# Kernel tuning notes

Measured on AMD Instinct MI355X. Metric: run time of the kernel, lower is better.

The kernel has to match this reference:

```python
import jax, jax.numpy as jnp
import numpy as np

B, N, C, K, H = 64, 4096, 256, 8, 256  # H = max(dim, hidden_dim=128)
ITERS = 3
EPS = 1e-8


def _ln(x, g, b):
    # torch LayerNorm: biased variance, eps=1e-5
    m = x.mean(-1, keepdims=True)
    v = ((x - m) ** 2).mean(-1, keepdims=True)
    return (x - m) * jax.lax.rsqrt(v + 1e-5) * g + b


def setup_inputs() -> dict:
    key = jax.random.key(0)
    ks = jax.random.split(key, 16)
    s = 0.02
    d = {}
    d['inputs'] = jax.random.normal(ks[0], (B, N, C), jnp.float32)
    d['slots_noise'] = jax.random.normal(ks[1], (K, C), jnp.float32)  # eval-mode shared noise
    d['mu'] = jax.random.normal(ks[2], (C,), jnp.float32)
    d['log_sigma'] = jax.random.normal(ks[3], (C,), jnp.float32) * 0.1
    d['ln_in_g'] = jnp.ones((C,), jnp.float32); d['ln_in_b'] = jnp.zeros((C,), jnp.float32)
    d['ln_s_g'] = jnp.ones((C,), jnp.float32); d['ln_s_b'] = jnp.zeros((C,), jnp.float32)
    d['ln_ff_g'] = jnp.ones((C,), jnp.float32); d['ln_ff_b'] = jnp.zeros((C,), jnp.float32)
    d['Wq'] = jax.random.normal(ks[4], (C, C), jnp.float32) * s; d['bq'] = jnp.zeros((C,), jnp.float32)
    d['Wk'] = jax.random.normal(ks[5], (C, C), jnp.float32) * s; d['bk'] = jnp.zeros((C,), jnp.float32)
    d['Wv'] = jax.random.normal(ks[6], (C, C), jnp.float32) * s; d['bv'] = jnp.zeros((C,), jnp.float32)
    d['W_ih'] = jax.random.normal(ks[7], (C, 3 * C), jnp.float32) * s; d['b_ih'] = jnp.zeros((3 * C,), jnp.float32)
    d['W_hh'] = jax.random.normal(ks[8], (C, 3 * C), jnp.float32) * s; d['b_hh'] = jnp.zeros((3 * C,), jnp.float32)
    d['W1'] = jax.random.normal(ks[9], (C, H), jnp.float32) * s; d['b1'] = jnp.zeros((H,), jnp.float32)
    d['W2'] = jax.random.normal(ks[10], (H, C), jnp.float32) * s; d['b2'] = jnp.zeros((C,), jnp.float32)
    return d


def reference(inputs, slots_noise, mu, log_sigma,
              ln_in_g, ln_in_b, ln_s_g, ln_s_b, ln_ff_g, ln_ff_b,
              Wq, bq, Wk, bk, Wv, bv,
              W_ih, b_ih, W_hh, b_hh,
              W1, b1, W2, b2):
    scale = C ** (-0.5)
    # eval-mode slot init: mu + exp(log_sigma) * noise, shared across batch
    slots = jnp.broadcast_to(mu + jnp.exp(log_sigma) * slots_noise, (B, K, C))
    x = _ln(inputs, ln_in_g, ln_in_b)
    k = x @ Wk + bk  # [B,N,C]
    v = x @ Wv + bv  # [B,N,C]
    for _ in range(ITERS):
        slots_prev = slots
        sn = _ln(slots, ln_s_g, ln_s_b)
        q = sn @ Wq + bq  # [B,K,C]
        dots = jnp.einsum('bid,bjd->bij', q, k) * scale  # [B,K,N]
        attn = jax.nn.softmax(dots, axis=1) + EPS  # softmax over slots (queries)
        attn = attn / attn.sum(-1, keepdims=True)  # renormalize over keys
        updates = jnp.einsum('bjd,bij->bid', v, attn)  # [B,K,C]
        # torch GRUCell
        gx = updates @ W_ih + b_ih
        gh = slots_prev @ W_hh + b_hh
        xr, xz, xn = jnp.split(gx, 3, axis=-1)
        hr, hz, hn = jnp.split(gh, 3, axis=-1)
        r = jax.nn.sigmoid(xr + hr)
        z = jax.nn.sigmoid(xz + hz)
        n = jnp.tanh(xn + r * hn)
        slots = (1.0 - z) * n + z * slots_prev
        pre = _ln(slots, ln_ff_g, ln_ff_b)
        slots = slots + (jax.nn.relu(pre @ W1 + b1) @ W2 + b2)
    return slots
```

## Files before the change

### kernel.cpp

```cpp
#include <hip/hip_runtime.h>
#include <hip/hip_bf16.h>

#define B_ 64
#define N_ 4096
#define C_ 256
#define K_ 8
#define M_ (B_*N_)
#define ITERS_ 3
#define SCALE_ 0.0625f
#define EPS_ 1e-8f

typedef __attribute__((ext_vector_type(4))) float f32x4;
typedef __attribute__((ext_vector_type(8))) __bf16 bf16x8;
typedef __attribute__((ext_vector_type(8))) unsigned short ushort8;
typedef __attribute__((ext_vector_type(4))) unsigned short ushort4v;

static __device__ __forceinline__ unsigned short f2bf(float f){
    union { float f; unsigned u; } v; v.f = f;
    unsigned r = v.u + 0x7fffu + ((v.u >> 16) & 1u);
    return (unsigned short)(r >> 16);
}
static __device__ __forceinline__ float bf2f(unsigned short h){
    union { unsigned u; float f; } v; v.u = ((unsigned)h) << 16;
    return v.f;
}

__global__ void prep1_kernel(const float* __restrict__ mu, const float* __restrict__ lsig,
                             const float* __restrict__ noise, float* __restrict__ slots){
    int idx = blockIdx.x*256 + threadIdx.x;
    int c = idx & 255, i = (idx >> 8) & 7;
    slots[idx] = mu[c] + expf(lsig[c])*noise[i*256 + c];
}

__global__ void prep2_kernel(const float* __restrict__ Wq, const float* __restrict__ Wk,
                             const float* __restrict__ bq, const float* __restrict__ bk,
                             float* __restrict__ WqkT, float* __restrict__ bqt,
                             float* __restrict__ wqb, float* __restrict__ bqkv){
    __shared__ float wqrow[256], bkl[256], bql[256];
    __shared__ float red[4], red2[4];
    const int t = threadIdx.x, c = blockIdx.x;
    wqrow[t] = Wq[(size_t)c*256 + t];
    bkl[t] = bk[t];
    bql[t] = bq[t];
    __syncthreads();
    float acc = 0.f, accb = 0.f;
    const float* wkr = Wk + (size_t)t*256;
    #pragma unroll 4
    for (int d = 0; d < 256; d += 4){
        float4 wk4 = *(const float4*)(wkr + d);
        float4 wq4 = *(const float4*)(&wqrow[d]);
        float4 bq4 = *(const float4*)(&bql[d]);
        acc  += wq4.x*wk4.x + wq4.y*wk4.y + wq4.z*wk4.z + wq4.w*wk4.w;
        accb += bq4.x*wk4.x + bq4.y*wk4.y + bq4.z*wk4.z + bq4.w*wk4.w;
    }
    WqkT[(size_t)c*256 + t] = acc;
    if (c == 0) bqt[t] = accb;
    float pw = wqrow[t]*bkl[t];
    float pb = bql[t]*bkl[t];
    #pragma unroll
    for (int m = 1; m < 64; m <<= 1){ pw += __shfl_xor(pw, m); pb += __shfl_xor(pb, m); }
    if ((t & 63) == 0){ red[t >> 6] = pw; red2[t >> 6] = pb; }
    __syncthreads();
    if (t == 0){
        wqb[c] = red[0] + red[1] + red[2] + red[3];
        if (c == 0) bqkv[0] = red2[0] + red2[1] + red2[2] + red2[3];
    }
}

__global__ void ln_kernel(const float* __restrict__ x, const float* __restrict__ g,
                          const float* __restrict__ bta, unsigned short* __restrict__ XH){
    const int t = threadIdx.x;
    const int row = blockIdx.x*32 + (t >> 3), sl = t & 7;
    const float* xr = x + (size_t)row*C_ + sl*32;
    float v[32];
    #pragma unroll
    for (int q = 0; q < 8; ++q) *(float4*)&v[q*4] = *(const float4*)(xr + q*4);
    float sum = 0.f, sq = 0.f;
    #pragma unroll
    for (int e = 0; e < 32; ++e){ sum += v[e]; sq += v[e]*v[e]; }
    #pragma unroll
    for (int m = 1; m < 8; m <<= 1){ sum += __shfl_xor(sum, m); sq += __shfl_xor(sq, m); }
    float mean = sum * (1.f/256.f);
    float rstd = rsqrtf(sq * (1.f/256.f) - mean*mean + 1e-5f);
    const int jt = row >> 8, rloc = row & 255;
    unsigned short* dst = XH + (((size_t)jt*8 + sl)*256 + rloc)*32;
    #pragma unroll
    for (int u = 0; u < 4; ++u){
        float4 g0 = *(const float4*)(g + sl*32 + u*8);
        float4 g1 = *(const float4*)(g + sl*32 + u*8 + 4);
        float4 b0 = *(const float4*)(bta + sl*32 + u*8);
        float4 b1 = *(const float4*)(bta + sl*32 + u*8 + 4);
        const float* gp0 = (const float*)&g0; const float* gp1 = (const float*)&g1;
        const float* bp0 = (const float*)&b0; const float* bp1 = (const float*)&b1;
        ushort8 pk;
        #pragma unroll
        for (int e = 0; e < 4; ++e){
            pk[e]   = f2bf((v[u*8+e]   - mean)*rstd*gp0[e] + bp0[e]);
            pk[4+e] = f2bf((v[u*8+4+e] - mean)*rstd*gp1[e] + bp1[e]);
        }
        *(ushort8*)(dst + u*8) = pk;
    }
}

__global__ void slotq_kernel(const float* __restrict__ slots, const float* __restrict__ WqkT,
                             const float* __restrict__ bqt, const float* __restrict__ wqb,
                             const float* __restrict__ bqkv, const float* __restrict__ gs,
                             const float* __restrict__ bs, float* __restrict__ qtbuf,
                             float* __restrict__ qbb){
    __shared__ float sn[8][260];
    const int t = threadIdx.x, b = blockIdx.x, cgb = blockIdx.y;
    const int i = t >> 6, l = t & 63;
    {
        float4 v4 = *(const float4*)(slots + ((size_t)b*8 + i)*256 + l*4);
        float sum = v4.x + v4.y + v4.z + v4.w;
        float sq  = v4.x*v4.x + v4.y*v4.y + v4.z*v4.z + v4.w*v4.w;
        #pragma unroll
        for (int m = 1; m < 64; m <<= 1){ sum += __shfl_xor(sum, m); sq += __shfl_xor(sq, m); }
        float mean = sum * (1.f/256.f);
        float rstd = rsqrtf(sq * (1.f/256.f) - mean*mean + 1e-5f);
        float4 g4 = *(const float4*)(gs + l*4);
        float4 b4 = *(const float4*)(bs + l*4);
        float n0 = (v4.x - mean)*rstd*g4.x + b4.x;
        float n1 = (v4.y - mean)*rstd*g4.y + b4.y;
        float n2 = (v4.z - mean)*rstd*g4.z + b4.z;
        float n3 = (v4.w - mean)*rstd*g4.w + b4.w;
        sn[i][l*4+0] = n0; sn[i][l*4+1] = n1; sn[i][l*4+2] = n2; sn[i][l*4+3] = n3;
        if (cgb == 0){
            float4 w4 = *(const float4*)(wqb + l*4);
            float pb = n0*w4.x + n1*w4.y + n2*w4.z + n3*w4.w;
            #pragma unroll
            for (int m = 1; m < 64; m <<= 1) pb += __shfl_xor(pb, m);
            if (l == 0) qbb[(size_t)b*8 + i] = SCALE_*(pb + bqkv[0]);
        }
    }
    __syncthreads();
    const int col = cgb*64 + l;
    float acc = bqt[col];
    #pragma unroll
    for (int cb = 0; cb < 256; cb += 64){
        float w[64];
        #pragma unroll
        for (int u = 0; u < 64; ++u) w[u] = WqkT[(size_t)(cb+u)*256 + col];
        #pragma unroll
        for (int u = 0; u < 64; ++u) acc += sn[i][cb+u]*w[u];
    }
    qtbuf[((size_t)b*8 + i)*256 + col] = SCALE_*acc;
}

__global__ void attn_kernel(const unsigned short* __restrict__ XH, const float* __restrict__ qt,
                            const float* __restrict__ qb, float* __restrict__ Spart,
                            float* __restrict__ Upart){
    __shared__ __align__(16) unsigned short xs[2*8192];
    __shared__ __align__(16) unsigned short pst[16*40];
    __shared__ float swred[2][8];
    const int t = threadIdx.x, b = blockIdx.x, jb = blockIdx.y;
    const unsigned short* XB = XH + (size_t)(b*16 + jb)*65536;
    const int wv = t >> 6, l = t & 63;
    const int bi = l & 15, kg = l >> 4;

    bf16x8 bfrag[8];
    float qbl = 0.f;
    {
        const ushort8 zz = (ushort8){0,0,0,0,0,0,0,0};
        #pragma unroll
        for (int ks = 0; ks < 8; ++ks) bfrag[ks] = __builtin_bit_cast(bf16x8, zz);
        if (wv < 2 && bi < 8){
            #pragma unroll
            for (int ks = 0; ks < 8; ++ks){
                const float* qp = qt + ((size_t)b*8 + bi)*256 + ks*32 + kg*8;
                float4 qa = *(const float4*)qp;
                float4 qc = *(const float4*)(qp + 4);
                ushort8 pk;
                pk[0]=f2bf(qa.x); pk[1]=f2bf(qa.y); pk[2]=f2bf(qa.z); pk[3]=f2bf(qa.w);
                pk[4]=f2bf(qc.x); pk[5]=f2bf(qc.y); pk[6]=f2bf(qc.z); pk[7]=f2bf(qc.w);
                bfrag[ks] = __builtin_bit_cast(bf16x8, pk);
            }
            qbl = qb[(size_t)b*8 + bi];
        }
    }

    const int og = t >> 5, r = t & 31;
    const int swr = (r & 7) ^ (((r >> 3) & 3) << 1);
    ushort8 s0, s1, s2, s3;
    {
        const unsigned short* g0 = XB + ((size_t)og*256 + r)*32;
        s0 = *(const ushort8*)(g0);      s1 = *(const ushort8*)(g0 + 8);
        s2 = *(const ushort8*)(g0 + 16); s3 = *(const ushort8*)(g0 + 24);
    }
    {
        unsigned short* xw = &xs[r*256];
        *(ushort8*)&xw[((og*4 + 0) ^ swr)*8] = s0;
        *(ushort8*)&xw[((og*4 + 1) ^ swr)*8] = s1;
        *(ushort8*)&xw[((og*4 + 2) ^ swr)*8] = s2;
        *(ushort8*)&xw[((og*4 + 3) ^ swr)*8] = s3;
    }
    __syncthreads();

    f32x4 acc[4];
    #pragma unroll
    for (int n = 0; n < 4; ++n) acc[n] = (f32x4){0.f,0.f,0.f,0.f};
    float s8loc = 0.f;
    const int pv_lo = bi & 7;
    const int pv_sl = (bi >> 3) ^ (kg << 1);

    for (int ch = 0; ch < 8; ++ch){
        const int cur = (ch & 1) << 13;
        if (ch < 7){
            const unsigned short* g1 = XB + ((size_t)og*256 + (ch+1)*32 + r)*32;
            s0 = *(const ushort8*)(g1);      s1 = *(const ushort8*)(g1 + 8);
            s2 = *(const ushort8*)(g1 + 16); s3 = *(const ushort8*)(g1 + 24);
        }
        if (wv < 2){
            f32x4 qacc = (f32x4){0.f,0.f,0.f,0.f};
            const int rowL = wv*16 + bi;
            const int swrow = (rowL & 7) ^ (((rowL >> 3) & 3) << 1);
            const unsigned short* xrow = &xs[cur + rowL*256];
            #pragma unroll
            for (int ks = 0; ks < 8; ++ks){
                int chn = (ks*4 + kg) ^ swrow;
                bf16x8 af = *(const bf16x8*)&xrow[chn*8];
                qacc = __builtin_amdgcn_mfma_f32_16x16x32_bf16(af, bfrag[ks], qacc, 0, 0, 0);
            }
            ushort4v p4;
            #pragma unroll
            for (int rr = 0; rr < 4; ++rr){
                float d = qacc[rr] + qbl;
                float mx = d;
                mx = fmaxf(mx, __shfl_xor(mx, 1));
                mx = fmaxf(mx, __shfl_xor(mx, 2));
                mx = fmaxf(mx, __shfl_xor(mx, 4));
                float e = __expf(d - mx);
                float se = e;
                se += __shfl_xor(se, 1);
                se += __shfl_xor(se, 2);
                se += __shfl_xor(se, 4);
                float p = e/se + EPS_;
                p4[rr] = f2bf(p);
                if (bi < 8) s8loc += p;
            }
            if (bi < 8)
                *(ushort4v*)&pst[bi*40 + wv*16 + kg*4] = p4;
        }
        if (ch < 7){
            unsigned short* xw = &xs[(cur ^ 8192) + r*256];
            *(ushort8*)&xw[((og*4 + 0) ^ swr)*8] = s0;
            *(ushort8*)&xw[((og*4 + 1) ^ swr)*8] = s1;
            *(ushort8*)&xw[((og*4 + 2) ^ swr)*8] = s2;
            *(ushort8*)&xw[((og*4 + 3) ^ swr)*8] = s3;
        }
        __syncthreads();
        {
            ushort8 pa = *(const ushort8*)&pst[bi*40 + kg*8];
            #pragma unroll
            for (int n = 0; n < 4; ++n){
                const int ct2 = (wv*4 + n) << 1;
                ushort8 xv;
                #pragma unroll
                for (int e = 0; e < 8; ++e){
                    int slot = (ct2 ^ pv_sl ^ e) ^ ((e & 4) ? 0 : 0);
                    xv[e] = xs[cur + kg*2048 + e*256 + (slot << 3) + pv_lo];
                }
                acc[n] = __builtin_amdgcn_mfma_f32_16x16x32_bf16(
                    __builtin_bit_cast(bf16x8, pa), __builtin_bit_cast(bf16x8, xv), acc[n], 0, 0, 0);
            }
        }
        __syncthreads();
    }
    if (wv < 2){
        s8loc += __shfl_xor(s8loc, 16);
        s8loc += __shfl_xor(s8loc, 32);
        if (l < 8) swred[wv][l] = s8loc;
    }
    __syncthreads();
    if (t < 8)
        Spart[((size_t)(b*16 + jb))*8 + t] = swred[0][t] + swred[1][t];
    if (kg < 2){
        #pragma unroll
        for (int n = 0; n < 4; ++n){
            const int ct = wv*4 + n;
            #pragma unroll
            for (int r2 = 0; r2 < 4; ++r2){
                int i = kg*4 + r2;
                Upart[(((size_t)(b*16 + jb))*8 + i)*256 + ct*16 + bi] = acc[n][r2];
            }
        }
    }
}

__global__ void slotu1_kernel(const float* __restrict__ slots, const float* __restrict__ Spart,
                              const float* __restrict__ Upart, const float* __restrict__ Wv,
                              const float* __restrict__ bv, const float* __restrict__ W_ih,
                              const float* __restrict__ b_ih, const float* __restrict__ W_hh,
                              const float* __restrict__ b_hh, float* __restrict__ slots2){
    __shared__ float us[8][260], sp[8][260], upd[8][260];
    const int t = threadIdx.x, b = blockIdx.x, ng = blockIdx.y;
    const int i = t >> 6, l = t & 63;
    {
        float a0 = 0.f, a1 = 0.f, a2 = 0.f, a3 = 0.f, S = 0.f;
        #pragma unroll
        for (int jbl = 0; jbl < 16; ++jbl){
            float4 u4 = *(const float4*)(Upart + (((size_t)(b*16 + jbl))*8 + i)*256 + l*4);
            a0 += u4.x; a1 += u4.y; a2 += u4.z; a3 += u4.w;
            S += Spart[((size_t)(b*16 + jbl))*8 + i];
        }
        float invS = 1.f / S;
        us[i][l*4+0] = a0*invS; us[i][l*4+1] = a1*invS;
        us[i][l*4+2] = a2*invS; us[i][l*4+3] = a3*invS;
        float4 s4 = *(const float4*)(slots + ((size_t)b*8 + i)*256 + l*4);
        sp[i][l*4+0] = s4.x; sp[i][l*4+1] = s4.y; sp[i][l*4+2] = s4.z; sp[i][l*4+3] = s4.w;
    }
    __syncthreads();
    {
        const int c4 = l*4;
        float4 acc = *(const float4*)(bv + c4);
        #pragma unroll
        for (int cb = 0; cb < 256; cb += 16){
            float4 w4[16];
            #pragma unroll
            for (int u = 0; u < 16; ++u)
                w4[u] = *(const float4*)(Wv + (size_t)(cb+u)*256 + c4);
            #pragma unroll
            for (int u = 0; u < 16; ++u){
                float uv = us[i][cb+u];
                acc.x += uv*w4[u].x; acc.y += uv*w4[u].y;
                acc.z += uv*w4[u].z; acc.w += uv*w4[u].w;
            }
        }
        *(float4*)&upd[i][c4] = acc;
    }
    __syncthreads();
    {
        const int n = ng*64 + l;
        float xr = b_ih[n], xz = b_ih[256+n], xn = b_ih[512+n];
        float hr = b_hh[n], hz = b_hh[256+n], hn = b_hh[512+n];
        #pragma unroll 2
        for (int cb = 0; cb < 256; cb += 8){
            float wi0[8], wi1[8], wi2[8], wh0[8], wh1[8], wh2[8];
            #pragma unroll
            for (int u = 0; u < 8; ++u){
                const float* wi = W_ih + (size_t)(cb+u)*768 + n;
                const float* wh = W_hh + (size_t)(cb+u)*768 + n;
                wi0[u] = wi[0]; wi1[u] = wi[256]; wi2[u] = wi[512];
                wh0[u] = wh[0]; wh1[u] = wh[256]; wh2[u] = wh[512];
            }
            #pragma unroll
            for (int u = 0; u < 8; ++u){
                float uv = upd[i][cb+u], sv = sp[i][cb+u];
                xr += uv*wi0[u]; xz += uv*wi1[u]; xn += uv*wi2[u];
                hr += sv*wh0[u]; hz += sv*wh1[u]; hn += sv*wh2[u];
            }
        }
        float rv = 1.f/(1.f + __expf(-(xr + hr)));
        float zv = 1.f/(1.f + __expf(-(xz + hz)));
        float nn = tanhf(xn + rv*hn);
        slots2[((size_t)b*8 + i)*256 + n] = (1.f - zv)*nn + zv*sp[i][n];
    }
}

__global__ void slotu2_kernel(const float* __restrict__ slots2, const float* __restrict__ gf,
                              const float* __restrict__ bf, const float* __restrict__ W1,
                              const float* __restrict__ b1, const float* __restrict__ W2,
                              const float* __restrict__ b2, float* __restrict__ slots,
                              float* __restrict__ dout){
    __shared__ float s0[8][260], pre[8][260], hb[8][260];
    const int t = threadIdx.x, b = blockIdx.x, ng = blockIdx.y;
    const int i = t >> 6, l = t & 63;
    {
        float4 v4 = *(const float4*)(slots2 + ((size_t)b*8 + i)*256 + l*4);
        float sum = v4.x + v4.y + v4.z + v4.w;
        float sq  = v4.x*v4.x + v4.y*v4.y + v4.z*v4.z + v4.w*v4.w;
        #pragma unroll
        for (int m = 1; m < 64; m <<= 1){ sum += __shfl_xor(sum, m); sq += __shfl_xor(sq, m); }
        float mean = sum * (1.f/256.f);
        float rstd = rsqrtf(sq * (1.f/256.f) - mean*mean + 1e-5f);
        float4 g4 = *(const float4*)(gf + l*4);
        float4 b4 = *(const float4*)(bf + l*4);
        s0[i][l*4+0] = v4.x; s0[i][l*4+1] = v4.y; s0[i][l*4+2] = v4.z; s0[i][l*4+3] = v4.w;
        pre[i][l*4+0] = (v4.x - mean)*rstd*g4.x + b4.x;
        pre[i][l*4+1] = (v4.y - mean)*rstd*g4.y + b4.y;
        pre[i][l*4+2] = (v4.z - mean)*rstd*g4.z + b4.z;
        pre[i][l*4+3] = (v4.w - mean)*rstd*g4.w + b4.w;
    }
    __syncthreads();
    {
        const int h4 = l*4;
        float4 acc = *(const float4*)(b1 + h4);
        #pragma unroll
        for (int cb = 0; cb < 256; cb += 16){
            float4 w4[16];
            #pragma unroll
            for (int u = 0; u < 16; ++u)
                w4[u] = *(const float4*)(W1 + (size_t)(cb+u)*256 + h4);
            #pragma unroll
            for (int u = 0; u < 16; ++u){
                float pv = pre[i][cb+u];
                acc.x += pv*w4[u].x; acc.y += pv*w4[u].y;
                acc.z += pv*w4[u].z; acc.w += pv*w4[u].w;
            }
        }
        hb[i][h4+0] = fmaxf(acc.x, 0.f); hb[i][h4+1] = fmaxf(acc.y, 0.f);
        hb[i][h4+2] = fmaxf(acc.z, 0.f); hb[i][h4+3] = fmaxf(acc.w, 0.f);
    }
    __syncthreads();
    {
        const int n = ng*64 + l;
        float acc = b2[n];
        #pragma unroll
        for (int mb = 0; mb < 256; mb += 64){
            float w[64];
            #pragma unroll
            for (int u = 0; u < 64; ++u) w[u] = W2[(size_t)(mb+u)*256 + n];
            #pragma unroll
            for (int u = 0; u < 64; ++u) acc += hb[i][mb+u]*w[u];
        }
        float val = s0[i][n] + acc;
        size_t off = ((size_t)b*8 + i)*256 + n;
        slots[off] = val;
        dout[off]  = val;
    }
}

extern "C" void kernel_launch(void* const* d_in, const int* in_sizes, int n_in,
                              void* d_out, int out_size, void* d_ws, size_t ws_size,
                              hipStream_t stream){
    const float* inputs = (const float*)d_in[0];
    const float* noise  = (const float*)d_in[1];
    const float* mu     = (const float*)d_in[2];
    const float* lsig   = (const float*)d_in[3];
    const float* g_in   = (const float*)d_in[4];
    const float* b_in   = (const float*)d_in[5];
    const float* g_s    = (const float*)d_in[6];
    const float* b_s    = (const float*)d_in[7];
    const float* g_ff   = (const float*)d_in[8];
    const float* b_ff   = (const float*)d_in[9];
    const float* Wq     = (const float*)d_in[10];
    const float* bq     = (const float*)d_in[11];
    const float* Wk     = (const float*)d_in[12];
    const float* bk     = (const float*)d_in[13];
    const float* Wv     = (const float*)d_in[14];
    const float* bv     = (const float*)d_in[15];
    const float* W_ih   = (const float*)d_in[16];
    const float* b_ih   = (const float*)d_in[17];
    const float* W_hh   = (const float*)d_in[18];
    const float* b_hh   = (const float*)d_in[19];
    const float* W1     = (const float*)d_in[20];
    const float* b1     = (const float*)d_in[21];
    const float* W2     = (const float*)d_in[22];
    const float* b2     = (const float*)d_in[23];

    char* ws = (char*)d_ws;
    unsigned short* XH  = (unsigned short*)(ws);
    float* Upart        = (float*)(ws + ((size_t)128 << 20));
    float* Spart        = (float*)(ws + ((size_t)136 << 20));
    float* qtbuf        = (float*)(ws + ((size_t)137 << 20));
    float* qbb          = (float*)(ws + ((size_t)138 << 20));
    float* slots        = (float*)(ws + ((size_t)139 << 20));
    float* slots2       = (float*)(ws + ((size_t)140 << 20));
    float* WqkT         = (float*)(ws + ((size_t)141 << 20));
    float* bqt          = (float*)(ws + ((size_t)142 << 20));
    float* wqb          = (float*)(ws + ((size_t)143 << 20));
    float* bqkv         = (float*)(ws + ((size_t)144 << 20));

    prep1_kernel<<<512, 256, 0, stream>>>(mu, lsig, noise, slots);
    prep2_kernel<<<256, 256, 0, stream>>>(Wq, Wk, bq, bk, WqkT, bqt, wqb, bqkv);
    ln_kernel<<<M_/32, 256, 0, stream>>>(inputs, g_in, b_in, XH);
    for (int it = 0; it < ITERS_; ++it){
        slotq_kernel<<<dim3(B_, 4), 512, 0, stream>>>(slots, WqkT, bqt, wqb, bqkv,
                                                      g_s, b_s, qtbuf, qbb);
        attn_kernel<<<dim3(B_, 16), 256, 0, stream>>>(XH, qtbuf, qbb, Spart, Upart);
        slotu1_kernel<<<dim3(B_, 4), 512, 0, stream>>>(slots, Spart, Upart, Wv, bv,
                                                       W_ih, b_ih, W_hh, b_hh, slots2);
        slotu2_kernel<<<dim3(B_, 4), 512, 0, stream>>>(slots2, g_ff, b_ff, W1, b1, W2, b2,
                                                       slots, (float*)d_out);
    }
}
```

Measured before the change: 530.2 us.

## Warp-specialize attention kernel into load, QK-softmax, and PV roles with pipelining

The attention kernel now runs 512 threads split into three wave roles: two waves do QK plus softmax, two waves stage X chunks from global memory into a 4-deep LDS ring, and four waves do the PV MMA one chunk behind. The earlier version had every wave alternate between loading, QK and PV with two barriers per chunk. The new schedule has one barrier per step and overlaps global loads, QK and PV across consecutive chunks. It doubles LDS use and thread count per block, which may lower occupancy, and leaves the QK and staging waves idle during some phases.

```diff
diff --git a/kernel.cpp b/kernel.cpp
--- a/kernel.cpp
+++ b/kernel.cpp
@@ -147,16 +147,18 @@
     qtbuf[((size_t)b*8 + i)*256 + col] = SCALE_*acc;
 }
 
-__global__ void attn_kernel(const unsigned short* __restrict__ XH, const float* __restrict__ qt,
-                            const float* __restrict__ qb, float* __restrict__ Spart,
-                            float* __restrict__ Upart){
-    __shared__ __align__(16) unsigned short xs[2*8192];
-    __shared__ __align__(16) unsigned short pst[16*40];
+__global__ __launch_bounds__(512)
+void attn_kernel(const unsigned short* __restrict__ XH, const float* __restrict__ qt,
+                 const float* __restrict__ qb, float* __restrict__ Spart,
+                 float* __restrict__ Upart){
+    __shared__ __align__(16) unsigned short xs[4*8192];
+    __shared__ __align__(16) unsigned short pst[2][16*40];
     __shared__ float swred[2][8];
     const int t = threadIdx.x, b = blockIdx.x, jb = blockIdx.y;
     const unsigned short* XB = XH + (size_t)(b*16 + jb)*65536;
     const int wv = t >> 6, l = t & 63;
     const int bi = l & 15, kg = l >> 4;
+    const bool isQK = (wv < 2), isST = (wv == 2 || wv == 3), isPV = (wv >= 4);
 
     bf16x8 bfrag[8];
     float qbl = 0.f;
@@ -164,7 +166,7 @@
         const ushort8 zz = (ushort8){0,0,0,0,0,0,0,0};
         #pragma unroll
         for (int ks = 0; ks < 8; ++ks) bfrag[ks] = __builtin_bit_cast(bf16x8, zz);
-        if (wv < 2 && bi < 8){
+        if (isQK && bi < 8){
             #pragma unroll
             for (int ks = 0; ks < 8; ++ks){
                 const float* qp = qt + ((size_t)b*8 + bi)*256 + ks*32 + kg*8;
@@ -178,39 +180,54 @@
             qbl = qb[(size_t)b*8 + bi];
         }
     }
-
-    const int og = t >> 5, r = t & 31;
-    const int swr = (r & 7) ^ (((r >> 3) & 3) << 1);
-    ushort8 s0, s1, s2, s3;
-    {
-        const unsigned short* g0 = XB + ((size_t)og*256 + r)*32;
-        s0 = *(const ushort8*)(g0);      s1 = *(const ushort8*)(g0 + 8);
-        s2 = *(const ushort8*)(g0 + 16); s3 = *(const ushort8*)(g0 + 24);
-    }
-    {
-        unsigned short* xw = &xs[r*256];
-        *(ushort8*)&xw[((og*4 + 0) ^ swr)*8] = s0;
-        *(ushort8*)&xw[((og*4 + 1) ^ swr)*8] = s1;
-        *(ushort8*)&xw[((og*4 + 2) ^ swr)*8] = s2;
-        *(ushort8*)&xw[((og*4 + 3) ^ swr)*8] = s3;
-    }
-    __syncthreads();
-
+    const int rstg = (wv & 1)*16 + bi;
+    const int og0 = (l >> 4) * 2;
+    const int swrr = (rstg & 7) ^ (((rstg >> 3) & 3) << 1);
+    ushort8 S[8];
     f32x4 acc[4];
     #pragma unroll
     for (int n = 0; n < 4; ++n) acc[n] = (f32x4){0.f,0.f,0.f,0.f};
-    float s8loc = 0.f;
     const int pv_lo = bi & 7;
     const int pv_sl = (bi >> 3) ^ (kg << 1);
-
-    for (int ch = 0; ch < 8; ++ch){
-        const int cur = (ch & 1) << 13;
-        if (ch < 7){
-            const unsigned short* g1 = XB + ((size_t)og*256 + (ch+1)*32 + r)*32;
-            s0 = *(const ushort8*)(g1);      s1 = *(const ushort8*)(g1 + 8);
-            s2 = *(const ushort8*)(g1 + 16); s3 = *(const ushort8*)(g1 + 24);
-        }
-        if (wv < 2){
+    float s8loc = 0.f;
+
+#define STG_LOAD(ch) { \
+    _Pragma("unroll") for (int o2 = 0; o2 < 2; ++o2){ \
+        const unsigned short* gp = XB + ((size_t)(og0+o2)*256 + (ch)*32 + rstg)*32; \
+        _Pragma("unroll") for (int u = 0; u < 4; ++u) S[o2*4+u] = *(const ushort8*)(gp + u*8); } }
+#define STG_WRITE(ch) { \
+    unsigned short* xw = &xs[((ch)&3)*8192 + rstg*256]; \
+    _Pragma("unroll") for (int o2 = 0; o2 < 2; ++o2){ \
+        _Pragma("unroll") for (int u = 0; u < 4; ++u) \
+            *(ushort8*)&xw[((((og0+o2)*4 + u) ^ swrr)*8)] = S[o2*4+u]; } }
+#define BARR() { asm volatile("s_waitcnt lgkmcnt(0)" ::: "memory"); __builtin_amdgcn_s_barrier(); }
+
+    if (isST){
+        STG_LOAD(0); STG_WRITE(0);
+        STG_LOAD(1);
+    }
+    BARR();
+
+    #pragma unroll
+    for (int p = 0; p < 8; ++p){
+        if (isPV && p >= 1){
+            const int cur = ((p-1) & 3) * 8192;
+            ushort8 pa = *(const ushort8*)&pst[(p-1) & 1][bi*40 + kg*8];
+            #pragma unroll
+            for (int n = 0; n < 4; ++n){
+                const int ct2 = ((wv - 4)*4 + n) << 1;
+                ushort8 xv;
+                #pragma unroll
+                for (int e = 0; e < 8; ++e){
+                    int slot = ct2 ^ pv_sl ^ e;
+                    xv[e] = xs[cur + kg*2048 + e*256 + (slot << 3) + pv_lo];
+                }
+                acc[n] = __builtin_amdgcn_mfma_f32_16x16x32_bf16(
+                    __builtin_bit_cast(bf16x8, pa), __builtin_bit_cast(bf16x8, xv), acc[n], 0, 0, 0);
+            }
+        }
+        if (isQK){
+            const int cur = (p & 3) * 8192;
             f32x4 qacc = (f32x4){0.f,0.f,0.f,0.f};
             const int rowL = wv*16 + bi;
             const int swrow = (rowL & 7) ^ (((rowL >> 3) & 3) << 1);
@@ -234,50 +251,48 @@
                 se += __shfl_xor(se, 1);
                 se += __shfl_xor(se, 2);
                 se += __shfl_xor(se, 4);
-                float p = e/se + EPS_;
-                p4[rr] = f2bf(p);
-                if (bi < 8) s8loc += p;
+                float pv = e/se + EPS_;
+                p4[rr] = f2bf(pv);
+                if (bi < 8) s8loc += pv;
             }
             if (bi < 8)
-                *(ushort4v*)&pst[bi*40 + wv*16 + kg*4] = p4;
-        }
-        if (ch < 7){
-            unsigned short* xw = &xs[(cur ^ 8192) + r*256];
-            *(ushort8*)&xw[((og*4 + 0) ^ swr)*8] = s0;
-            *(ushort8*)&xw[((og*4 + 1) ^ swr)*8] = s1;
-            *(ushort8*)&xw[((og*4 + 2) ^ swr)*8] = s2;
-            *(ushort8*)&xw[((og*4 + 3) ^ swr)*8] = s3;
-        }
-        __syncthreads();
-        {
-            ushort8 pa = *(const ushort8*)&pst[bi*40 + kg*8];
-            #pragma unroll
-            for (int n = 0; n < 4; ++n){
-                const int ct2 = (wv*4 + n) << 1;
-                ushort8 xv;
-                #pragma unroll
-                for (int e = 0; e < 8; ++e){
-                    int slot = (ct2 ^ pv_sl ^ e) ^ ((e & 4) ? 0 : 0);
-                    xv[e] = xs[cur + kg*2048 + e*256 + (slot << 3) + pv_lo];
-                }
-                acc[n] = __builtin_amdgcn_mfma_f32_16x16x32_bf16(
-                    __builtin_bit_cast(bf16x8, pa), __builtin_bit_cast(bf16x8, xv), acc[n], 0, 0, 0);
-            }
-        }
-        __syncthreads();
-    }
-    if (wv < 2){
-        s8loc += __shfl_xor(s8loc, 16);
-        s8loc += __shfl_xor(s8loc, 32);
-        if (l < 8) swred[wv][l] = s8loc;
-    }
-    __syncthreads();
+                *(ushort4v*)&pst[p & 1][bi*40 + wv*16 + kg*4] = p4;
+        }
+        if (isST){
+            if (p + 1 <= 7) STG_WRITE(p + 1);
+            if (p + 2 <= 7) STG_LOAD(p + 2);
+        }
+        BARR();
+    }
+    if (isPV){
+        const int cur = (7 & 3) * 8192;
+        ushort8 pa = *(const ushort8*)&pst[7 & 1][bi*40 + kg*8];
+        #pragma unroll
+        for (int n = 0; n < 4; ++n){
+            const int ct2 = ((wv - 4)*4 + n) << 1;
+            ushort8 xv;
+            #pragma unroll
+            for (int e = 0; e < 8; ++e){
+                int slot = ct2 ^ pv_sl ^ e;
+                xv[e] = xs[cur + kg*2048 + e*256 + (slot << 3) + pv_lo];
+            }
+            acc[n] = __builtin_amdgcn_mfma_f32_16x16x32_bf16(
+                __builtin_bit_cast(bf16x8, pa), __builtin_bit_cast(bf16x8, xv), acc[n], 0, 0, 0);
+        }
+    }
+    if (isQK){
+        float s = s8loc;
+        s += __shfl_xor(s, 16);
+        s += __shfl_xor(s, 32);
+        if (l < 8) swred[wv][l] = s;
+    }
+    BARR();
     if (t < 8)
         Spart[((size_t)(b*16 + jb))*8 + t] = swred[0][t] + swred[1][t];
-    if (kg < 2){
+    if (isPV && kg < 2){
         #pragma unroll
         for (int n = 0; n < 4; ++n){
-            const int ct = wv*4 + n;
+            const int ct = (wv - 4)*4 + n;
             #pragma unroll
             for (int r2 = 0; r2 < 4; ++r2){
                 int i = kg*4 + r2;
@@ -285,6 +300,9 @@
             }
         }
     }
+#undef STG_LOAD
+#undef STG_WRITE
+#undef BARR
 }
 
 __global__ void slotu1_kernel(const float* __restrict__ slots, const float* __restrict__ Spart,
@@ -467,7 +485,7 @@
     for (int it = 0; it < ITERS_; ++it){
         slotq_kernel<<<dim3(B_, 4), 512, 0, stream>>>(slots, WqkT, bqt, wqb, bqkv,
                                                       g_s, b_s, qtbuf, qbb);
-        attn_kernel<<<dim3(B_, 16), 256, 0, stream>>>(XH, qtbuf, qbb, Spart, Upart);
+        attn_kernel<<<dim3(B_, 16), 512, 0, stream>>>(XH, qtbuf, qbb, Spart, Upart);
         slotu1_kernel<<<dim3(B_, 4), 512, 0, stream>>>(slots, Spart, Upart, Wv, bv,
                                                        W_ih, b_ih, W_hh, b_hh, slots2);
         slotu2_kernel<<<dim3(B_, 4), 512, 0, stream>>>(slots2, g_ff, b_ff, W1, b1, W2, b2,
```

Measured after the change: 513.1 us. 3.2% less time.
